# Kernel tuning notes

Measured on AMD Instinct MI355X. Metric: run time of the kernel, lower is better.

Reference implementation:

```python
import jax, jax.numpy as jnp
import numpy as np

N = 10000
E = 160000
D = 512
EPS = 1e-5


def _lin_params(key, out_d, in_d, bias=True):
    k1, k2 = jax.random.split(key)
    s = 1.0 / np.sqrt(in_d)
    W = jax.random.uniform(k1, (out_d, in_d), jnp.float32, -s, s)
    if bias:
        b = jax.random.uniform(k2, (out_d,), jnp.float32, -s, s)
        return W, b
    return (W,)


def setup_inputs() -> dict:
    key = jax.random.key(0)
    ks = jax.random.split(key, 16)
    inp = {
        "x": jax.random.normal(ks[0], (N, D), jnp.float32),
        "edge_index": jax.random.randint(ks[1], (2, E), 0, N, jnp.int64),
    }
    ki = 2
    for l in range(3):
        Wp, bp = _lin_params(ks[ki], D, D); ki += 1
        Wl, bl = _lin_params(ks[ki], D, D); ki += 1
        (Wr,) = _lin_params(ks[ki], D, D, bias=False); ki += 1
        inp[f"Wp{l}"] = Wp; inp[f"bp{l}"] = bp
        inp[f"Wl{l}"] = Wl; inp[f"bl{l}"] = bl
        inp[f"Wr{l}"] = Wr
        if l < 2:  # ReLU+LayerNorm between convs
            inp[f"g{l}"] = jnp.ones((D,), jnp.float32)
            inp[f"be{l}"] = jnp.zeros((D,), jnp.float32)
    return inp


def _sage_conv(x, src, dst, Wp, bp, Wl, bl, Wr):
    # PyG SAGEConv with project=True: project+ReLU messages, mean-aggregate, lin_l + lin_r(root)
    h = jax.nn.relu(x @ Wp.T + bp)                      # [N, D] projected messages
    agg = jax.ops.segment_sum(h[src], dst, num_segments=N)   # gather + scatter-add
    cnt = jax.ops.segment_sum(jnp.ones((src.shape[0],), x.dtype), dst, num_segments=N)
    agg = agg / jnp.maximum(cnt, 1.0)[:, None]          # mean over incoming edges
    return agg @ Wl.T + bl + x @ Wr.T


def _relu_ln(x, g, b):
    x = jax.nn.relu(x)
    mu = jnp.mean(x, axis=-1, keepdims=True)
    var = jnp.mean(jnp.square(x - mu), axis=-1, keepdims=True)
    return (x - mu) * jax.lax.rsqrt(var + EPS) * g + b


def reference(x, edge_index,
              Wp0, bp0, Wl0, bl0, Wr0, g0, be0,
              Wp1, bp1, Wl1, bl1, Wr1, g1, be1,
              Wp2, bp2, Wl2, bl2, Wr2):
    src, dst = edge_index[0], edge_index[1]
    x = _sage_conv(x, src, dst, Wp0, bp0, Wl0, bl0, Wr0)
    x = _relu_ln(x, g0, be0)
    x = _sage_conv(x, src, dst, Wp1, bp1, Wl1, bl1, Wr1)
    x = _relu_ln(x, g1, be1)
    x = _sage_conv(x, src, dst, Wp2, bp2, Wl2, bl2, Wr2)
    return x
```

## Files before the change

### kernel.cpp

```cpp
#include <hip/hip_runtime.h>
#include <cstdint>

#define D 512
#define TM 128
#define TN 64
#define BK 32
#define CAP 64

typedef unsigned short u16;
typedef __bf16 bf16x8 __attribute__((ext_vector_type(8)));
typedef float f32x4 __attribute__((ext_vector_type(4)));

__device__ __forceinline__ float bf2f(u16 u) {
    unsigned int x = ((unsigned int)u) << 16;
    return __builtin_bit_cast(float, x);
}
__device__ __forceinline__ u16 f2bf(float f) {
    unsigned int x = __builtin_bit_cast(unsigned int, f);
    x += 0x7fffu + ((x >> 16) & 1u);
    return (u16)(x >> 16);
}
__device__ __forceinline__ float loadf(const void* p, int i, bool bf) {
    return bf ? bf2f(((const u16*)p)[i]) : ((const float*)p)[i];
}
__device__ __forceinline__ void gload16(const u16* g, u16* l) {
    __builtin_amdgcn_global_load_lds(
        (const __attribute__((address_space(1))) void*)(uintptr_t)g,
        (__attribute__((address_space(3))) void*)(unsigned int)(uintptr_t)l,
        16, 0, 0);
}
__device__ __forceinline__ bool is_bf16(const u16* xraw) {
    int lane = threadIdx.x & 63;
    u16 u = xraw[2 * lane];
    int e = (u >> 7) & 0xFF;
    unsigned long long b = __ballot(e >= 110 && e <= 129);
    return __popcll(b) >= 32;
}
__device__ __forceinline__ bool is_i64(const int* eraw) {
    int lane = threadIdx.x & 63;
    unsigned long long b = __ballot(eraw[2 * lane + 1] == 0);
    return __popcll(b) >= 32;
}

struct PrepArgs {
    const u16* xraw; const int* eraw;
    const void* W[9];
    const void* V[10];
    u16* xb; u16* Wb; float* vecf;
    int* cnt; u16* bucket;
    int M, E;
};

__global__ __launch_bounds__(256) void prep(PrepArgs a)
{
    const bool bf  = is_bf16(a.xraw);
    const bool i64 = is_i64(a.eraw);
    const int gt = blockIdx.x * 256 + threadIdx.x;
    const int gs = gridDim.x * 256;

    const int nx = a.M * D / 8;
    for (int i = gt; i < nx; i += gs) {
        if (bf) {
            *(uint4*)(a.xb + i * 8) = *(const uint4*)(a.xraw + i * 8);
        } else {
            const float* f = (const float*)a.xraw + i * 8;
            float4 p = *(const float4*)f, q = *(const float4*)(f + 4);
            u16 r[8] = {f2bf(p.x), f2bf(p.y), f2bf(p.z), f2bf(p.w),
                        f2bf(q.x), f2bf(q.y), f2bf(q.z), f2bf(q.w)};
            *(uint4*)(a.xb + i * 8) = *(uint4*)r;
        }
    }

    for (int i = gt; i < 9 * 32768; i += gs) {
        int m = i >> 15, j = i & 32767;
        const void* gsrc = nullptr;
        if (m == 3 || m == 5) gsrc = a.V[2];
        else if (m == 6 || m == 8) gsrc = a.V[6];
        const void* src = a.W[m];
        int c0 = (j * 8) & 511;
        float v[8];
        if (bf) {
            const u16* s = (const u16*)src + j * 8;
#pragma unroll
            for (int e = 0; e < 8; e++) v[e] = bf2f(s[e]);
        } else {
            const float* s = (const float*)src + j * 8;
#pragma unroll
            for (int e = 0; e < 8; e++) v[e] = s[e];
        }
        if (gsrc) {
#pragma unroll
            for (int e = 0; e < 8; e++) v[e] *= loadf(gsrc, c0 + e, bf);
        }
        u16 r[8];
#pragma unroll
        for (int e = 0; e < 8; e++) r[e] = f2bf(v[e]);
        *(uint4*)(a.Wb + (size_t)m * D * D + j * 8) = *(uint4*)r;
    }

    for (int e = gt; e < 10 * 512; e += gs) {
        int t = e >> 9, n = e & 511;
        float outv;
        if (t == 0)      outv = loadf(a.V[0], n, bf);
        else if (t == 1) outv = loadf(a.V[1], n, bf);
        else {
            int q = t - 2;
            const int wi[8] = {3, 3, 5, 5, 6, 6, 8, 8};
            const void* wraw = a.W[wi[q]];
            const void* dotv = (q < 4) ? ((q & 1) ? a.V[3] : a.V[2])
                                       : ((q & 1) ? a.V[7] : a.V[6]);
            float acc = 0.f;
            if (bf) {
                const u16* wr = (const u16*)wraw + (size_t)n * 512;
                for (int k = 0; k < 512; k++) acc += bf2f(wr[k]) * loadf(dotv, k, bf);
            } else {
                const float* wr = (const float*)wraw + (size_t)n * 512;
                for (int k = 0; k < 512; k++) acc += wr[k] * loadf(dotv, k, bf);
            }
            if (q & 1) {
                const void* braw = (q == 1) ? a.V[4] : (q == 3) ? a.V[5]
                                 : (q == 5) ? a.V[8] : a.V[9];
                acc += loadf(braw, n, bf);
            }
            outv = acc;
        }
        a.vecf[t * 512 + n] = outv;
    }

    for (int e2 = gt; e2 < a.E; e2 += gs) {
        int s, d;
        if (i64) { s = a.eraw[2 * e2]; d = a.eraw[2 * (a.E + e2)]; }
        else     { s = a.eraw[e2];     d = a.eraw[a.E + e2]; }
        s = min(max(s, 0), a.M - 1);
        d = min(max(d, 0), a.M - 1);
        int p = atomicAdd(&a.cnt[d], 1);
        if (p < CAP) a.bucket[(size_t)d * CAP + p] = (u16)s;
    }
}

template <bool LNIN>
__global__ __launch_bounds__(256) void gemm1k(
    const u16* __restrict__ A, const u16* __restrict__ W,
    const float* __restrict__ bias, const float* __restrict__ svec,
    const float* __restrict__ mu, const float* __restrict__ m2,
    u16* __restrict__ hout, int M)
{
    __shared__ __align__(16) u16 sA[TM * BK];
    __shared__ __align__(16) u16 sB[TN * BK];

    const int t    = threadIdx.x;
    const int m0   = blockIdx.x * TM;
    const int n0   = blockIdx.y * TN;
    const int wave = t >> 6, lane = t & 63;
    const int wm   = wave >> 1, wn = wave & 1;
    const int lrow = lane & 15, quad = lane >> 4;

    float rstd[4][4], nmu[4][4];
    if (LNIN) {
#pragma unroll
        for (int mi = 0; mi < 4; mi++)
#pragma unroll
            for (int r = 0; r < 4; r++) {
                int row = min(m0 + wm * 64 + mi * 16 + quad * 4 + r, M - 1);
                float mean = mu[row] * (1.f / 512.f);
                float var  = m2[row] * (1.f / 512.f) - mean * mean;
                float rs   = rsqrtf(fmaxf(var, 0.f) + 1e-5f);
                rstd[mi][r] = rs;
                nmu[mi][r]  = -mean * rs;
            }
    }

    f32x4 acc[4][2];
#pragma unroll
    for (int i = 0; i < 4; i++)
#pragma unroll
        for (int j = 0; j < 2; j++)
#pragma unroll
            for (int r = 0; r < 4; r++) acc[i][j][r] = 0.f;

    const int cA    = (t & 3) * 8;
    const int rowA0 = min(m0 + (t >> 2),      M - 1);
    const int rowA1 = min(m0 + 64 + (t >> 2), M - 1);
    const int rowB  = n0 + (t >> 2);
    const u16* gA0 = A + (size_t)rowA0 * D + cA;
    const u16* gA1 = A + (size_t)rowA1 * D + cA;
    const u16* gB  = W + (size_t)rowB  * D + cA;

#pragma unroll 1
    for (int k0 = 0; k0 < D; k0 += BK) {
        gload16(gA0 + k0, &sA[(size_t)t * 8]);
        gload16(gA1 + k0, &sA[(size_t)(t + 256) * 8]);
        gload16(gB  + k0, &sB[(size_t)t * 8]);
        __syncthreads();
        bf16x8 af[4], bfr[2];
#pragma unroll
        for (int mi = 0; mi < 4; mi++)
            af[mi] = *(const bf16x8*)&sA[(wm * 64 + mi * 16 + lrow) * BK + quad * 8];
#pragma unroll
        for (int ni = 0; ni < 2; ni++)
            bfr[ni] = *(const bf16x8*)&sB[(wn * 32 + ni * 16 + lrow) * BK + quad * 8];
#pragma unroll
        for (int mi = 0; mi < 4; mi++)
#pragma unroll
            for (int ni = 0; ni < 2; ni++)
                acc[mi][ni] = __builtin_amdgcn_mfma_f32_16x16x32_bf16(
                    af[mi], bfr[ni], acc[mi][ni], 0, 0, 0);
        __syncthreads();
    }

#pragma unroll
    for (int ni = 0; ni < 2; ni++) {
        int col = n0 + wn * 32 + ni * 16 + lrow;
        float bv = bias[col];
        float sv = LNIN ? svec[col] : 0.f;
#pragma unroll
        for (int mi = 0; mi < 4; mi++) {
            int row0 = m0 + wm * 64 + mi * 16 + quad * 4;
#pragma unroll
            for (int r = 0; r < 4; r++) {
                int row = row0 + r;
                if (row < M) {
                    float v = LNIN ? rstd[mi][r] * acc[mi][ni][r] + nmu[mi][r] * sv + bv
                                   : acc[mi][ni][r] + bv;
                    hout[(size_t)row * D + col] = f2bf(fmaxf(v, 0.f));
                }
            }
        }
    }
}

template <bool LNIN, bool STATS, bool FINAL>
__global__ __launch_bounds__(256) void gemm2k(
    const u16* __restrict__ A0, const u16* __restrict__ W0,
    const u16* __restrict__ A1, const u16* __restrict__ W1,
    const float* __restrict__ bias, const float* __restrict__ s2vec,
    const float* __restrict__ mu_in, const float* __restrict__ m2_in,
    float* __restrict__ mu_out, float* __restrict__ m2_out,
    void* __restrict__ out, const u16* __restrict__ xraw, int M)
{
    __shared__ __align__(16) u16 sA[TM * BK];
    __shared__ __align__(16) u16 sB[TN * BK];

    const int t    = threadIdx.x;
    const int m0   = blockIdx.x * TM;
    const int n0   = blockIdx.y * TN;
    const int wave = t >> 6, lane = t & 63;
    const int wm   = wave >> 1, wn = wave & 1;
    const int lrow = lane & 15, quad = lane >> 4;

    const bool out_bf16 = FINAL ? is_bf16(xraw) : true;

    float rstd[4][4], nmu[4][4], inv[4][4];
    if (LNIN) {
#pragma unroll
        for (int mi = 0; mi < 4; mi++)
#pragma unroll
            for (int r = 0; r < 4; r++) {
                int row = min(m0 + wm * 64 + mi * 16 + quad * 4 + r, M - 1);
                float mean = mu_in[row] * (1.f / 512.f);
                float var  = m2_in[row] * (1.f / 512.f) - mean * mean;
                float s    = sqrtf(fmaxf(var, 0.f) + 1e-5f);
                float rs   = 1.f / s;
                rstd[mi][r] = rs;
                inv[mi][r]  = s;
                nmu[mi][r]  = -mean * rs;
            }
    }

    f32x4 acc[4][2];
#pragma unroll
    for (int i = 0; i < 4; i++)
#pragma unroll
        for (int j = 0; j < 2; j++)
#pragma unroll
            for (int r = 0; r < 4; r++) acc[i][j][r] = 0.f;

    const int cA    = (t & 3) * 8;
    const int rowA0 = min(m0 + (t >> 2),      M - 1);
    const int rowA1 = min(m0 + 64 + (t >> 2), M - 1);
    const int rowB  = n0 + (t >> 2);

#pragma unroll 1
    for (int p = 0; p < 2; p++) {
        const u16* A = p ? A1 : A0;
        const u16* W = p ? W1 : W0;
        if (LNIN && p == 1) {
#pragma unroll
            for (int mi = 0; mi < 4; mi++)
#pragma unroll
                for (int ni = 0; ni < 2; ni++)
#pragma unroll
                    for (int r = 0; r < 4; r++) acc[mi][ni][r] *= inv[mi][r];
        }
        const u16* gA0 = A + (size_t)rowA0 * D + cA;
        const u16* gA1 = A + (size_t)rowA1 * D + cA;
        const u16* gB  = W + (size_t)rowB  * D + cA;

#pragma unroll 1
        for (int k0 = 0; k0 < D; k0 += BK) {
            gload16(gA0 + k0, &sA[(size_t)t * 8]);
            gload16(gA1 + k0, &sA[(size_t)(t + 256) * 8]);
            gload16(gB  + k0, &sB[(size_t)t * 8]);
            __syncthreads();
            bf16x8 af[4], bfr[2];
#pragma unroll
            for (int mi = 0; mi < 4; mi++)
                af[mi] = *(const bf16x8*)&sA[(wm * 64 + mi * 16 + lrow) * BK + quad * 8];
#pragma unroll
            for (int ni = 0; ni < 2; ni++)
                bfr[ni] = *(const bf16x8*)&sB[(wn * 32 + ni * 16 + lrow) * BK + quad * 8];
#pragma unroll
            for (int mi = 0; mi < 4; mi++)
#pragma unroll
                for (int ni = 0; ni < 2; ni++)
                    acc[mi][ni] = __builtin_amdgcn_mfma_f32_16x16x32_bf16(
                        af[mi], bfr[ni], acc[mi][ni], 0, 0, 0);
            __syncthreads();
        }
    }

    float bvv[2], svv[2];
#pragma unroll
    for (int ni = 0; ni < 2; ni++) {
        int col = n0 + wn * 32 + ni * 16 + lrow;
        bvv[ni] = bias[col];
        svv[ni] = LNIN ? s2vec[col] : 0.f;
    }

#pragma unroll
    for (int mi = 0; mi < 4; mi++) {
#pragma unroll
        for (int r = 0; r < 4; r++) {
            int row = m0 + wm * 64 + mi * 16 + quad * 4 + r;
            float sr = 0.f, s2r = 0.f;
#pragma unroll
            for (int ni = 0; ni < 2; ni++) {
                int col = n0 + wn * 32 + ni * 16 + lrow;
                float v = acc[mi][ni][r];
                if (LNIN) v = rstd[mi][r] * v + nmu[mi][r] * svv[ni] + bvv[ni];
                else      v += bvv[ni];
                if (FINAL) {
                    if (row < M) {
                        if (out_bf16) ((u16*)out)[(size_t)row * D + col] = f2bf(v);
                        else          ((float*)out)[(size_t)row * D + col] = v;
                    }
                } else {
                    u16 zb = f2bf(fmaxf(v, 0.f));
                    float z = bf2f(zb);
                    if (row < M) ((u16*)out)[(size_t)row * D + col] = zb;
                    sr  += z;
                    s2r += z * z;
                }
            }
            if (STATS) {
#pragma unroll
                for (int off = 1; off <= 8; off <<= 1) {
                    sr  += __shfl_xor(sr, off);
                    s2r += __shfl_xor(s2r, off);
                }
                if (lrow == 0 && row < M) {
                    atomicAdd(&mu_out[row], sr);
                    atomicAdd(&m2_out[row], s2r);
                }
            }
        }
    }
}

__global__ __launch_bounds__(256) void aggregate(
    const u16* __restrict__ h, const int* __restrict__ cnt,
    const u16* __restrict__ bucket, u16* __restrict__ agg, int M)
{
    const int w = threadIdx.x >> 6, lane = threadIdx.x & 63;
    const int n = blockIdx.x * 4 + w;

    __shared__ u16 sidx[4][CAP];
    int deg = 0, dd = 0;
    if (n < M) {
        deg = cnt[n];
        dd  = min(deg, CAP);
        if (lane < dd) sidx[w][lane] = bucket[(size_t)n * CAP + lane];
    }
    __syncthreads();
    if (n >= M) return;

    float a[8] = {0.f, 0.f, 0.f, 0.f, 0.f, 0.f, 0.f, 0.f};
    int i = 0;
    for (; i + 4 <= dd; i += 4) {
        uint4 v0 = *(const uint4*)(h + (size_t)sidx[w][i]     * D + lane * 8);
        uint4 v1 = *(const uint4*)(h + (size_t)sidx[w][i + 1] * D + lane * 8);
        uint4 v2 = *(const uint4*)(h + (size_t)sidx[w][i + 2] * D + lane * 8);
        uint4 v3 = *(const uint4*)(h + (size_t)sidx[w][i + 3] * D + lane * 8);
        const unsigned int* u0 = (const unsigned int*)&v0;
        const unsigned int* u1 = (const unsigned int*)&v1;
        const unsigned int* u2 = (const unsigned int*)&v2;
        const unsigned int* u3 = (const unsigned int*)&v3;
#pragma unroll
        for (int j = 0; j < 4; j++) {
            a[2 * j]     += bf2f((u16)(u0[j] & 0xffffu)) + bf2f((u16)(u1[j] & 0xffffu))
                          + bf2f((u16)(u2[j] & 0xffffu)) + bf2f((u16)(u3[j] & 0xffffu));
            a[2 * j + 1] += bf2f((u16)(u0[j] >> 16)) + bf2f((u16)(u1[j] >> 16))
                          + bf2f((u16)(u2[j] >> 16)) + bf2f((u16)(u3[j] >> 16));
        }
    }
    for (; i < dd; i++) {
        uint4 v0 = *(const uint4*)(h + (size_t)sidx[w][i] * D + lane * 8);
        const unsigned int* u0 = (const unsigned int*)&v0;
#pragma unroll
        for (int j = 0; j < 4; j++) {
            a[2 * j]     += bf2f((u16)(u0[j] & 0xffffu));
            a[2 * j + 1] += bf2f((u16)(u0[j] >> 16));
        }
    }

    float invd = 1.f / fmaxf((float)deg, 1.f);
    u16 r[8];
#pragma unroll
    for (int j = 0; j < 8; j++) r[j] = f2bf(a[j] * invd);
    *(uint4*)(agg + (size_t)n * D + lane * 8) = *(uint4*)r;
}

extern "C" void kernel_launch(void* const* d_in, const int* in_sizes, int n_in,
                              void* d_out, int out_size, void* d_ws, size_t ws_size,
                              hipStream_t stream)
{
    const int M = in_sizes[0] / D;
    const int E = in_sizes[1] / 2;

    PrepArgs a;
    a.xraw = (const u16*)d_in[0];
    a.eraw = (const int*)d_in[1];
    {
        int idx = 2;
        for (int l = 0; l < 3; l++) {
            a.W[l * 3 + 0] = d_in[idx++];
            a.V[l * 4 + 0] = d_in[idx++];
            a.W[l * 3 + 1] = d_in[idx++];
            a.V[l * 4 + 1] = d_in[idx++];
            a.W[l * 3 + 2] = d_in[idx++];
            if (l < 2) {
                a.V[l * 4 + 2] = d_in[idx++];
                a.V[l * 4 + 3] = d_in[idx++];
            }
        }
    }

    char* w = (char*)d_ws;
    auto alloc = [&](size_t bytes) { void* p = w; w += (bytes + 255) & ~(size_t)255; return p; };
    u16*   xb   = (u16*)  alloc((size_t)M * D * 2);
    u16*   h    = (u16*)  alloc((size_t)M * D * 2);
    u16*   aggb = (u16*)  alloc((size_t)M * D * 2);
    u16*   z0   = (u16*)  alloc((size_t)M * D * 2);
    u16*   z1   = (u16*)  alloc((size_t)M * D * 2);
    u16*   Wb   = (u16*)  alloc((size_t)9 * D * D * 2);
    float* vecf = (float*)alloc((size_t)10 * 512 * 4);
    int*   cnt  = (int*)  alloc((size_t)M * 4);
    float* mu0  = (float*)alloc((size_t)M * 4);
    float* m20  = (float*)alloc((size_t)M * 4);
    float* mu1  = (float*)alloc((size_t)M * 4);
    float* m21  = (float*)alloc((size_t)M * 4);
    u16* bucket = (u16*)  alloc((size_t)M * CAP * 2);

    a.xb = xb; a.Wb = Wb; a.vecf = vecf; a.cnt = cnt; a.bucket = bucket;
    a.M = M; a.E = E;

    hipMemsetAsync(cnt, 0, (size_t)((char*)bucket - (char*)cnt), stream);
    prep<<<dim3(1024), dim3(256), 0, stream>>>(a);

    const size_t DD = (size_t)D * D;
    dim3 gg((M + TM - 1) / TM, D / TN);
    dim3 ga((M + 3) / 4);

    gemm1k<false><<<gg, dim3(256), 0, stream>>>(
        xb, Wb + 0 * DD, vecf + 0 * 512, nullptr, nullptr, nullptr, h, M);
    aggregate<<<ga, dim3(256), 0, stream>>>(h, cnt, bucket, aggb, M);
    gemm2k<false, true, false><<<gg, dim3(256), 0, stream>>>(
        aggb, Wb + 1 * DD, xb, Wb + 2 * DD, vecf + 1 * 512, nullptr,
        nullptr, nullptr, mu0, m20, z0, a.xraw, M);

    gemm1k<true><<<gg, dim3(256), 0, stream>>>(
        z0, Wb + 3 * DD, vecf + 3 * 512, vecf + 2 * 512, mu0, m20, h, M);
    aggregate<<<ga, dim3(256), 0, stream>>>(h, cnt, bucket, aggb, M);
    gemm2k<true, true, false><<<gg, dim3(256), 0, stream>>>(
        aggb, Wb + 4 * DD, z0, Wb + 5 * DD, vecf + 5 * 512, vecf + 4 * 512,
        mu0, m20, mu1, m21, z1, a.xraw, M);

    gemm1k<true><<<gg, dim3(256), 0, stream>>>(
        z1, Wb + 6 * DD, vecf + 7 * 512, vecf + 6 * 512, mu1, m21, h, M);
    aggregate<<<ga, dim3(256), 0, stream>>>(h, cnt, bucket, aggb, M);
    gemm2k<true, false, true><<<gg, dim3(256), 0, stream>>>(
        aggb, Wb + 7 * DD, z1, Wb + 8 * DD, vecf + 9 * 512, vecf + 8 * 512,
        mu1, m21, nullptr, nullptr, d_out, a.xraw, M);
}
```

Measured before the change: 368.3 us.

## Double-buffer LDS tiles in GEMM kernels to overlap global loads with MFMA

Measured after the change: 365.2 us. No clear change (-0.8%).

```diff
diff --git a/kernel.cpp b/kernel.cpp
--- a/kernel.cpp
+++ b/kernel.cpp
@@ -28,6 +28,9 @@
         (const __attribute__((address_space(1))) void*)(uintptr_t)g,
         (__attribute__((address_space(3))) void*)(unsigned int)(uintptr_t)l,
         16, 0, 0);
+}
+__device__ __forceinline__ void drain_vm() {
+    asm volatile("s_waitcnt vmcnt(0)" ::: "memory");
 }
 __device__ __forceinline__ bool is_bf16(const u16* xraw) {
     int lane = threadIdx.x & 63;
@@ -145,8 +148,8 @@
     const float* __restrict__ mu, const float* __restrict__ m2,
     u16* __restrict__ hout, int M)
 {
-    __shared__ __align__(16) u16 sA[TM * BK];
-    __shared__ __align__(16) u16 sB[TN * BK];
+    __shared__ __align__(16) u16 sA[2][TM * BK];
+    __shared__ __align__(16) u16 sB[2][TN * BK];
 
     const int t    = threadIdx.x;
     const int m0   = blockIdx.x * TM;
@@ -186,26 +189,35 @@
     const u16* gA1 = A + (size_t)rowA1 * D + cA;
     const u16* gB  = W + (size_t)rowB  * D + cA;
 
+    gload16(gA0, &sA[0][(size_t)t * 8]);
+    gload16(gA1, &sA[0][(size_t)(t + 256) * 8]);
+    gload16(gB,  &sB[0][(size_t)t * 8]);
+
 #pragma unroll 1
     for (int k0 = 0; k0 < D; k0 += BK) {
-        gload16(gA0 + k0, &sA[(size_t)t * 8]);
-        gload16(gA1 + k0, &sA[(size_t)(t + 256) * 8]);
-        gload16(gB  + k0, &sB[(size_t)t * 8]);
+        const int it  = k0 >> 5;
+        const int cur = it & 1, nxt = cur ^ 1;
+        drain_vm();
         __syncthreads();
+        const int k1 = k0 + BK;
+        if (k1 < D) {
+            gload16(gA0 + k1, &sA[nxt][(size_t)t * 8]);
+            gload16(gA1 + k1, &sA[nxt][(size_t)(t + 256) * 8]);
+            gload16(gB  + k1, &sB[nxt][(size_t)t * 8]);
+        }
         bf16x8 af[4], bfr[2];
 #pragma unroll
         for (int mi = 0; mi < 4; mi++)
-            af[mi] = *(const bf16x8*)&sA[(wm * 64 + mi * 16 + lrow) * BK + quad * 8];
+            af[mi] = *(const bf16x8*)&sA[cur][(wm * 64 + mi * 16 + lrow) * BK + quad * 8];
 #pragma unroll
         for (int ni = 0; ni < 2; ni++)
-            bfr[ni] = *(const bf16x8*)&sB[(wn * 32 + ni * 16 + lrow) * BK + quad * 8];
+            bfr[ni] = *(const bf16x8*)&sB[cur][(wn * 32 + ni * 16 + lrow) * BK + quad * 8];
 #pragma unroll
         for (int mi = 0; mi < 4; mi++)
 #pragma unroll
             for (int ni = 0; ni < 2; ni++)
                 acc[mi][ni] = __builtin_amdgcn_mfma_f32_16x16x32_bf16(
                     af[mi], bfr[ni], acc[mi][ni], 0, 0, 0);
-        __syncthreads();
     }
 
 #pragma unroll
@@ -238,8 +250,8 @@
     float* __restrict__ mu_out, float* __restrict__ m2_out,
     void* __restrict__ out, const u16* __restrict__ xraw, int M)
 {
-    __shared__ __align__(16) u16 sA[TM * BK];
-    __shared__ __align__(16) u16 sB[TN * BK];
+    __shared__ __align__(16) u16 sA[2][TM * BK];
+    __shared__ __align__(16) u16 sB[2][TN * BK];
 
     const int t    = threadIdx.x;
     const int m0   = blockIdx.x * TM;
@@ -280,11 +292,26 @@
     const int rowA1 = min(m0 + 64 + (t >> 2), M - 1);
     const int rowB  = n0 + (t >> 2);
 
+    gload16(A0 + (size_t)rowA0 * D + cA, &sA[0][(size_t)t * 8]);
+    gload16(A0 + (size_t)rowA1 * D + cA, &sA[0][(size_t)(t + 256) * 8]);
+    gload16(W0 + (size_t)rowB  * D + cA, &sB[0][(size_t)t * 8]);
+
 #pragma unroll 1
-    for (int p = 0; p < 2; p++) {
-        const u16* A = p ? A1 : A0;
-        const u16* W = p ? W1 : W0;
-        if (LNIN && p == 1) {
+    for (int kk = 0; kk < 2 * D; kk += BK) {
+        const int it  = kk >> 5;
+        const int cur = it & 1, nxt = cur ^ 1;
+        drain_vm();
+        __syncthreads();
+        const int kn = kk + BK;
+        if (kn < 2 * D) {
+            const u16* A = (kn >= D) ? A1 : A0;
+            const u16* W = (kn >= D) ? W1 : W0;
+            const int k = kn & (D - 1);
+            gload16(A + (size_t)rowA0 * D + k + cA, &sA[nxt][(size_t)t * 8]);
+            gload16(A + (size_t)rowA1 * D + k + cA, &sA[nxt][(size_t)(t + 256) * 8]);
+            gload16(W + (size_t)rowB  * D + k + cA, &sB[nxt][(size_t)t * 8]);
+        }
+        if (LNIN && kk == D) {
 #pragma unroll
             for (int mi = 0; mi < 4; mi++)
 #pragma unroll
@@ -292,31 +319,19 @@
 #pragma unroll
                     for (int r = 0; r < 4; r++) acc[mi][ni][r] *= inv[mi][r];
         }
-        const u16* gA0 = A + (size_t)rowA0 * D + cA;
-        const u16* gA1 = A + (size_t)rowA1 * D + cA;
-        const u16* gB  = W + (size_t)rowB  * D + cA;
-
-#pragma unroll 1
-        for (int k0 = 0; k0 < D; k0 += BK) {
-            gload16(gA0 + k0, &sA[(size_t)t * 8]);
-            gload16(gA1 + k0, &sA[(size_t)(t + 256) * 8]);
-            gload16(gB  + k0, &sB[(size_t)t * 8]);
-            __syncthreads();
-            bf16x8 af[4], bfr[2];
-#pragma unroll
-            for (int mi = 0; mi < 4; mi++)
-                af[mi] = *(const bf16x8*)&sA[(wm * 64 + mi * 16 + lrow) * BK + quad * 8];
+        bf16x8 af[4], bfr[2];
+#pragma unroll
+        for (int mi = 0; mi < 4; mi++)
+            af[mi] = *(const bf16x8*)&sA[cur][(wm * 64 + mi * 16 + lrow) * BK + quad * 8];
+#pragma unroll
+        for (int ni = 0; ni < 2; ni++)
+            bfr[ni] = *(const bf16x8*)&sB[cur][(wn * 32 + ni * 16 + lrow) * BK + quad * 8];
+#pragma unroll
+        for (int mi = 0; mi < 4; mi++)
 #pragma unroll
             for (int ni = 0; ni < 2; ni++)
-                bfr[ni] = *(const bf16x8*)&sB[(wn * 32 + ni * 16 + lrow) * BK + quad * 8];
-#pragma unroll
-            for (int mi = 0; mi < 4; mi++)
-#pragma unroll
-                for (int ni = 0; ni < 2; ni++)
-                    acc[mi][ni] = __builtin_amdgcn_mfma_f32_16x16x32_bf16(
-                        af[mi], bfr[ni], acc[mi][ni], 0, 0, 0);
-            __syncthreads();
-        }
+                acc[mi][ni] = __builtin_amdgcn_mfma_f32_16x16x32_bf16(
+                    af[mi], bfr[ni], acc[mi][ni], 0, 0, 0);
     }
 
     float bvv[2], svv[2];
```
